# Kernel tuning notes

Hardware: AMD Instinct MI355X
Metric: run time of the kernel (lower is better)

## Reference

```python
import jax, jax.numpy as jnp
import numpy as np

N, K, E, H, I = 8192, 2, 8, 2048, 1408


def setup_inputs() -> dict:
    key = jax.random.key(0)
    k1, k2, k3, k4, k5 = jax.random.split(key, 5)
    x = jax.random.normal(k1, (N, H), dtype=jnp.float32)
    topk_indices = jax.random.randint(k2, (N, K), 0, E, dtype=jnp.int32)
    topk_weights = jax.random.uniform(k3, (N, K), dtype=jnp.float32)
    # normalize routing weights per token (typical top-k softmax output scale)
    topk_weights = topk_weights / jnp.sum(topk_weights, axis=-1, keepdims=True)
    scale = 0.02  # typical init std, keeps activations well-scaled
    gate_up_proj = jax.random.normal(k4, (E, H, 2 * I), dtype=jnp.float32) * scale
    down_proj = jax.random.normal(k5, (E, I, H), dtype=jnp.float32) * scale
    return {"x": x, "topk_indices": topk_indices, "topk_weights": topk_weights,
            "gate_up_proj": gate_up_proj, "down_proj": down_proj}


def reference(x, topk_indices, topk_weights, gate_up_proj, down_proj):
    """MoE experts: route -> grouped GEMM SwiGLU -> grouped GEMM -> weighted unroute.

    x: [N, H]; topk_indices/topk_weights: [N, K];
    gate_up_proj: [E, H, 2I]; down_proj: [E, I, H].
    """
    n, k = topk_indices.shape
    e = gate_up_proj.shape[0]
    flat_e = topk_indices.reshape(-1)                 # [N*K] expert id per routed slot
    sort_idx = jnp.argsort(flat_e)                    # stable sort: group slots by expert
    token_idx = sort_idx // k                         # source token for each sorted slot
    sorted_tokens = x[token_idx]                      # [N*K, H]
    group_sizes = jnp.bincount(flat_e, length=e).astype(jnp.int32)  # [E]
    # grouped (ragged) GEMM over contiguous expert groups
    h = jax.lax.ragged_dot(sorted_tokens, gate_up_proj, group_sizes)  # [N*K, 2I]
    gate_h, up_h = jnp.split(h, 2, axis=-1)
    intermediate = jax.nn.silu(gate_h) * up_h          # fused SwiGLU
    out_sorted = jax.lax.ragged_dot(intermediate, down_proj, group_sizes)  # [N*K, H]
    # weighted scatter-combine back to token order
    w_sorted = topk_weights.reshape(-1)[sort_idx]      # [N*K]
    out = jnp.zeros_like(x).at[token_idx].add(out_sorted * w_sorted[:, None])
    return out
```

## Files before the change

kernel.cpp:

```cpp
#include <hip/hip_runtime.h>


#define N_TOK 8192
#define TOPK  2
#define NEXP  8
#define HD    2048
#define ID    1408
#define NK    (N_TOK * TOPK)
#define NT256 (NK / 256 + NEXP)

typedef __bf16 bf16x8 __attribute__((ext_vector_type(8)));
typedef float  f32x4  __attribute__((ext_vector_type(4)));

__device__ __forceinline__ float b2f(unsigned short u) {
    union { unsigned int i; float f; } v; v.i = ((unsigned int)u) << 16; return v.f;
}
__device__ __forceinline__ unsigned short f2b(float f) {
    union { float f; unsigned int i; } v; v.f = f;
    unsigned int x = v.i;
    return (unsigned short)((x + 0x7fffu + ((x >> 16) & 1u)) >> 16);
}

__device__ __forceinline__ void glds16(const void* g, void* l) {
    __builtin_amdgcn_global_load_lds(
        (const __attribute__((address_space(1))) unsigned int*)g,
        (__attribute__((address_space(3))) unsigned int*)l,
        16, 0, 0);
}


__global__ void probe_k(const unsigned short* __restrict__ xu, int* __restrict__ mode) {
    __shared__ int c;
    if (threadIdx.x == 0) c = 0;
    __syncthreads();
    float a = fabsf(b2f(xu[threadIdx.x * 2]));
    int sane = (a > 1e-4f && a < 100.f) ? 1 : 0;
    atomicAdd(&c, sane);
    __syncthreads();
    if (threadIdx.x == 0) mode[0] = (c < 512) ? 1 : 0;
}


__global__ void convert_x(const void* __restrict__ x, unsigned short* __restrict__ xb,
                          const int* __restrict__ mode) {
    int gid = blockIdx.x * 256 + threadIdx.x;
    size_t o = (size_t)gid * 8;
    if (mode[0]) {
        const float* f = (const float*)x + o;
        float4 f0 = *(const float4*)f;
        float4 f1 = *(const float4*)(f + 4);
        uint4 v;
        v.x = f2b(f0.x) | ((unsigned int)f2b(f0.y) << 16);
        v.y = f2b(f0.z) | ((unsigned int)f2b(f0.w) << 16);
        v.z = f2b(f1.x) | ((unsigned int)f2b(f1.y) << 16);
        v.w = f2b(f1.z) | ((unsigned int)f2b(f1.w) << 16);
        *(uint4*)(xb + o) = v;
    } else {
        *(uint4*)(xb + o) = *(const uint4*)((const unsigned short*)x + o);
    }
}


__global__ void init_k(int* cnt, int* fill) {
    int t = threadIdx.x;
    if (t < NEXP) { cnt[t] = 0; fill[t] = 0; }
}

__global__ void route_count(const int* __restrict__ idx, int* __restrict__ cnt) {
    int s = blockIdx.x * 256 + threadIdx.x;
    if (s < NK) atomicAdd(&cnt[idx[s]], 1);
}

__global__ void route_scan(const int* __restrict__ cnt, int* __restrict__ base,
                           int* __restrict__ tb) {
    if (threadIdx.x == 0) {
        int acc = 0, tacc = 0;
        for (int e = 0; e < NEXP; e++) {
            base[e] = acc; tb[e] = tacc;
            acc += cnt[e]; tacc += (cnt[e] + 255) >> 8;
        }
        base[NEXP] = acc; tb[NEXP] = tacc;
    }
}

__global__ void route_scatter(const int* __restrict__ idx,
                              const int* __restrict__ base,
                              int* __restrict__ fill,
                              int* __restrict__ tok,
                              int* __restrict__ inv) {
    int s = blockIdx.x * 256 + threadIdx.x;
    if (s < NK) {
        int e = idx[s];
        int p = base[e] + atomicAdd(&fill[e], 1);
        tok[p] = s >> 1;
        inv[s] = p;
    }
}


__global__ void transpose_k(const void* __restrict__ in, unsigned short* __restrict__ out,
                            int R, int C, const int* __restrict__ mode) {
    __shared__ float tile[64][65];
    bool fp32m = (mode[0] != 0);
    int e  = blockIdx.z;
    int c0 = blockIdx.x * 64, r0 = blockIdx.y * 64;
    int t = threadIdx.x;
    if (fp32m) {
        const float* inp = (const float*)in + (size_t)e * R * C;
        for (int i = 0; i < 16; i++) {
            int lin = t + i * 256;
            int r = lin >> 6, c = lin & 63;
            tile[r][c] = inp[(size_t)(r0 + r) * C + c0 + c];
        }
    } else {
        const unsigned int* inp = (const unsigned int*)in + (size_t)e * R * (C >> 1);
        for (int i = 0; i < 8; i++) {
            int lin = t + i * 256;
            int r = lin >> 5, cu = lin & 31;
            unsigned int v = inp[(size_t)(r0 + r) * (C >> 1) + (c0 >> 1) + cu];
            tile[r][2 * cu]     = b2f((unsigned short)(v & 0xffffu));
            tile[r][2 * cu + 1] = b2f((unsigned short)(v >> 16));
        }
    }
    __syncthreads();
    unsigned int* outp = (unsigned int*)out + (size_t)e * C * (R >> 1);
    for (int i = 0; i < 8; i++) {
        int lin = t + i * 256;
        int c = lin >> 5, ru = lin & 31;
        unsigned int lo = f2b(tile[2 * ru][c]);
        unsigned int hi = f2b(tile[2 * ru + 1][c]);
        outp[(size_t)(c0 + c) * (R >> 1) + (r0 >> 1) + ru] = lo | (hi << 16);
    }
}



template<int KD, int ND, int LDA, bool GATHER>
__launch_bounds__(512, 2)
__global__ void gemm8_k(const unsigned short* __restrict__ A,
                        const unsigned short* __restrict__ B,
                        const int* __restrict__ base,
                        const int* __restrict__ tb,
                        const int* __restrict__ tok,
                        unsigned short* __restrict__ C) {
    extern __shared__ unsigned short lds[];
    const int CT = ND / 256;
    const int KT = KD / 64;
    int G = gridDim.x;
    int orig = blockIdx.x;
    int q8 = G >> 3, r8 = G & 7, xcd = orig & 7, lin = orig >> 3;
    int wgid = (xcd < r8 ? xcd * (q8 + 1) : r8 * (q8 + 1) + (xcd - r8) * q8) + lin;
    int ct  = wgid % CT;
    int rtf = wgid / CT;
    if (rtf >= tb[NEXP]) return;
    int e = 0;
    while (tb[e + 1] <= rtf) e++;
    int row0 = base[e] + (rtf - tb[e]) * 256;
    int rend = base[e + 1];

    int tid  = threadIdx.x;
    int lane = tid & 63;
    int wave = tid >> 6;
    int wm16 = (wave & 1) * 16;
    int wn16 = (wave >> 1) * 16;
    int l15 = lane & 15, qq = lane >> 4;
    int l7  = l15 & 7;

    const unsigned short* bbase = B + (size_t)e * ND * KD + (size_t)(ct * 256) * KD;

    const unsigned short* agp[2][2];
    const unsigned short* bgp[2][2];
    for (int j = 0; j < 2; j++) {
        int s = j * 512 + tid;
        int r = s >> 3;
        int c = (s & 7) ^ (r & 7);
        for (int h = 0; h < 2; h++) {
            int p = row0 + h * 128 + r;
            bool sv = (p < rend);
            const unsigned short* ar;
            if (GATHER) ar = sv ? A + (size_t)tok[p] * LDA : A;
            else        ar = sv ? A + (size_t)p * LDA      : A;
            agp[j][h] = ar + c * 8;
            bgp[j][h] = bbase + (size_t)(h * 128 + r) * KD + c * 8;
        }
    }
    int wbase = wave * 512;

    f32x4 acc[8][4];
#pragma unroll
    for (int m = 0; m < 8; m++)
#pragma unroll
        for (int n = 0; n < 4; n++) acc[m][n] = (f32x4){0.f, 0.f, 0.f, 0.f};

    bf16x8 af0[2], af1[2], bq[4][2];

#define STAGE_A(buf, h, kt) do { int _k = ((kt) < KT ? (kt) : KT - 1) * 64;     \
    glds16(agp[0][h] + _k, &lds[(buf) * 16384 + (h) * 8192 + wbase]);           \
    glds16(agp[1][h] + _k, &lds[(buf) * 16384 + (h) * 8192 + 4096 + wbase]); } while (0)
#define STAGE_B(buf, h, kt) do { int _k = ((kt) < KT ? (kt) : KT - 1) * 64;     \
    glds16(bgp[0][h] + _k, &lds[32768 + (buf) * 16384 + (h) * 8192 + wbase]);   \
    glds16(bgp[1][h] + _k, &lds[32768 + (buf) * 16384 + (h) * 8192 + 4096 + wbase]); } while (0)

#define ALDS(buf, m, ks) (*(const bf16x8*)&lds[(buf) * 16384 +                  \
    (((m) * 32 + wm16 + l15) * 8 + ((((ks) * 4) + qq) ^ l7)) * 8])
#define BLDS(buf, n, ks) (*(const bf16x8*)&lds[32768 + (buf) * 16384 +          \
    (((n) * 64 + wn16 + l15) * 8 + ((((ks) * 4) + qq) ^ l7)) * 8])

#define PH_READA(buf, m0)                                                       \
    af0[0] = ALDS(buf, m0, 0); af0[1] = ALDS(buf, m0, 1);                       \
    af1[0] = ALDS(buf, (m0) + 1, 0); af1[1] = ALDS(buf, (m0) + 1, 1);
#define PH_READB(buf)                                                           \
    _Pragma("unroll") for (int n = 0; n < 4; n++) {                             \
        bq[n][0] = BLDS(buf, n, 0); bq[n][1] = BLDS(buf, n, 1); }

#define MFMA16(m0) do {                                                         \
    _Pragma("unroll") for (int n = 0; n < 4; n++) {                             \
        acc[m0][n] = __builtin_amdgcn_mfma_f32_16x16x32_bf16(af0[0], bq[n][0], acc[m0][n], 0, 0, 0);         \
        acc[m0][n] = __builtin_amdgcn_mfma_f32_16x16x32_bf16(af0[1], bq[n][1], acc[m0][n], 0, 0, 0);         \
        acc[(m0) + 1][n] = __builtin_amdgcn_mfma_f32_16x16x32_bf16(af1[0], bq[n][0], acc[(m0) + 1][n], 0, 0, 0); \
        acc[(m0) + 1][n] = __builtin_amdgcn_mfma_f32_16x16x32_bf16(af1[1], bq[n][1], acc[(m0) + 1][n], 0, 0, 0); } } while (0)

#define SYNCA(m0)                                                               \
    __builtin_amdgcn_sched_barrier(0);                                          \
    __builtin_amdgcn_s_barrier();                                               \
    asm volatile("s_waitcnt lgkmcnt(0)" ::: "memory");                          \
    __builtin_amdgcn_sched_barrier(0);                                          \
    __builtin_amdgcn_s_setprio(1);                                              \
    MFMA16(m0);                                                                 \
    __builtin_amdgcn_s_setprio(0);                                              \
    __builtin_amdgcn_sched_barrier(0);                                          \
    __builtin_amdgcn_s_barrier();

#define SYNCV(m0)                                                               \
    __builtin_amdgcn_sched_barrier(0);                                          \
    asm volatile("s_waitcnt vmcnt(6)" ::: "memory");                            \
    __builtin_amdgcn_s_barrier();                                               \
    asm volatile("s_waitcnt lgkmcnt(0)" ::: "memory");                          \
    __builtin_amdgcn_sched_barrier(0);                                          \
    __builtin_amdgcn_s_setprio(1);                                              \
    MFMA16(m0);                                                                 \
    __builtin_amdgcn_s_setprio(0);                                              \
    __builtin_amdgcn_sched_barrier(0);                                          \
    __builtin_amdgcn_s_barrier();

    STAGE_A(0, 0, 0); STAGE_A(0, 1, 0); STAGE_B(0, 0, 0); STAGE_B(0, 1, 0);
    STAGE_B(1, 0, 1); STAGE_B(1, 1, 1); STAGE_A(1, 0, 1);
    __builtin_amdgcn_sched_barrier(0);
    asm volatile("s_waitcnt vmcnt(6)" ::: "memory");
    __builtin_amdgcn_s_barrier();
    __builtin_amdgcn_sched_barrier(0);

    for (int i = 0; i < KT / 2; i++) {
        int t1 = 2 * i + 1, t2 = 2 * i + 2, t3 = 2 * i + 3;
        PH_READB(0); PH_READA(0, 0); STAGE_A(1, 1, t1); SYNCA(0);
        PH_READA(0, 2);              STAGE_B(0, 0, t2); SYNCA(2);
        PH_READA(0, 4);              STAGE_B(0, 1, t2); SYNCA(4);
        PH_READA(0, 6);              STAGE_A(0, 0, t2); SYNCV(6);
        PH_READB(1); PH_READA(1, 0); STAGE_A(0, 1, t2); SYNCA(0);
        PH_READA(1, 2);              STAGE_B(1, 0, t3); SYNCA(2);
        PH_READA(1, 4);              STAGE_B(1, 1, t3); SYNCA(4);
        PH_READA(1, 6);              STAGE_A(1, 0, t3); SYNCV(6);
    }
    asm volatile("s_waitcnt vmcnt(0)" ::: "memory");

#undef STAGE_A
#undef STAGE_B
#undef ALDS
#undef BLDS
#undef PH_READA
#undef PH_READB
#undef MFMA16
#undef SYNCA
#undef SYNCV

#pragma unroll
    for (int m = 0; m < 8; m++) {
        int rbase = row0 + m * 32 + wm16 + qq * 4;
#pragma unroll
        for (int reg = 0; reg < 4; reg++) {
            int p = rbase + reg;
            if (p >= rend) continue;
#pragma unroll
            for (int n = 0; n < 4; n++) {
                int col = ct * 256 + n * 64 + wn16 + l15;
                C[(size_t)p * ND + col] = f2b(acc[m][n][reg]);
            }
        }
    }
}


__global__ void swiglu_k(unsigned short* __restrict__ h) {
    int gid = blockIdx.x * 256 + threadIdx.x;
    int row = gid / (ID / 8);
    int c8 = (gid - row * (ID / 8)) * 8;
    unsigned short* hr = h + (size_t)row * (2 * ID);
    uint4 gv = *(const uint4*)(hr + c8);
    uint4 uv = *(const uint4*)(hr + ID + c8);
    const unsigned short* ga = (const unsigned short*)&gv;
    const unsigned short* ua = (const unsigned short*)&uv;
    uint4 o;
    unsigned int* ro = (unsigned int*)&o;
    for (int i = 0; i < 4; i++) {
        float g0 = b2f(ga[2 * i]),     u0 = b2f(ua[2 * i]);
        float g1 = b2f(ga[2 * i + 1]), u1 = b2f(ua[2 * i + 1]);
        float s0 = (g0 / (1.f + __expf(-g0))) * u0;
        float s1 = (g1 / (1.f + __expf(-g1))) * u1;
        ro[i] = f2b(s0) | ((unsigned int)f2b(s1) << 16);
    }
    *(uint4*)(hr + c8) = o;
}


__global__ void combine_k(const unsigned short* __restrict__ outs,
                          const int* __restrict__ inv,
                          const void* __restrict__ w,
                          void* __restrict__ out,
                          const int* __restrict__ mode) {
    bool fp32m = (mode[0] != 0);
    int gid = blockIdx.x * 256 + threadIdx.x;
    int t  = gid >> 8;
    int c8 = (gid & 255) * 8;
    int p0 = inv[t * 2], p1 = inv[t * 2 + 1];
    float w0, w1;
    if (fp32m) {
        const float* wf = (const float*)w;
        w0 = wf[t * 2]; w1 = wf[t * 2 + 1];
    } else {
        const unsigned short* wu = (const unsigned short*)w;
        w0 = b2f(wu[t * 2]); w1 = b2f(wu[t * 2 + 1]);
    }
    uint4 v0 = *(const uint4*)(outs + (size_t)p0 * HD + c8);
    uint4 v1 = *(const uint4*)(outs + (size_t)p1 * HD + c8);
    const unsigned short* a = (const unsigned short*)&v0;
    const unsigned short* b = (const unsigned short*)&v1;
    float r[8];
    for (int i = 0; i < 8; i++) r[i] = w0 * b2f(a[i]) + w1 * b2f(b[i]);
    if (fp32m) {
        float* of = (float*)out + (size_t)t * HD + c8;
        *(float4*)of       = make_float4(r[0], r[1], r[2], r[3]);
        *(float4*)(of + 4) = make_float4(r[4], r[5], r[6], r[7]);
    } else {
        uint4 o;
        unsigned int* ro = (unsigned int*)&o;
        for (int i = 0; i < 4; i++)
            ro[i] = f2b(r[2 * i]) | ((unsigned int)f2b(r[2 * i + 1]) << 16);
        *(uint4*)((unsigned short*)out + (size_t)t * HD + c8) = o;
    }
}


extern "C" void kernel_launch(void* const* d_in, const int* in_sizes, int n_in,
                              void* d_out, int out_size, void* d_ws, size_t ws_size,
                              hipStream_t stream) {
    const void* x   = d_in[0];
    const int*  idx = (const int*)d_in[1];
    const void* w   = d_in[2];
    const void* gup = d_in[3];
    const void* dwn = d_in[4];

    char* ws = (char*)d_ws;
    int* mode = (int*)(ws);
    int* cnt  = (int*)(ws + 64);
    int* base = (int*)(ws + 128);
    int* fill = (int*)(ws + 192);
    int* tb   = (int*)(ws + 256);
    int* tok  = (int*)(ws + 512);
    int* inv  = (int*)(ws + 512 + 4 * NK);
    unsigned short* h    = (unsigned short*)(ws + 262144);
    unsigned short* xb   = h    + (size_t)NK * 2 * ID;
    unsigned short* dwnT = xb   + (size_t)N_TOK * HD;
    unsigned short* gupT = dwnT + (size_t)NEXP * HD * ID;
    unsigned short* outs = gupT;

    static bool attr_done = false;
    if (!attr_done) {
        hipFuncSetAttribute(
            reinterpret_cast<const void*>(&gemm8_k<HD, 2 * ID, HD, true>),
            hipFuncAttributeMaxDynamicSharedMemorySize, 131072);
        hipFuncSetAttribute(
            reinterpret_cast<const void*>(&gemm8_k<ID, HD, 2 * ID, false>),
            hipFuncAttributeMaxDynamicSharedMemorySize, 131072);
        attr_done = true;
    }

    probe_k<<<1, 1024, 0, stream>>>((const unsigned short*)x, mode);
    convert_x<<<(N_TOK * HD / 8) / 256, 256, 0, stream>>>(x, xb, mode);

    init_k<<<1, 64, 0, stream>>>(cnt, fill);
    route_count<<<NK / 256, 256, 0, stream>>>(idx, cnt);
    route_scan<<<1, 64, 0, stream>>>(cnt, base, tb);
    route_scatter<<<NK / 256, 256, 0, stream>>>(idx, base, fill, tok, inv);

    transpose_k<<<dim3(2 * ID / 64, HD / 64, NEXP), 256, 0, stream>>>(
        gup, gupT, HD, 2 * ID, mode);
    transpose_k<<<dim3(HD / 64, ID / 64, NEXP), 256, 0, stream>>>(
        dwn, dwnT, ID, HD, mode);

    gemm8_k<HD, 2 * ID, HD, true>
        <<<NT256 * (2 * ID / 256), 512, 131072, stream>>>(xb, gupT, base, tb, tok, h);
    swiglu_k<<<(NK * (ID / 8)) / 256, 256, 0, stream>>>(h);
    gemm8_k<ID, HD, 2 * ID, false>
        <<<NT256 * (HD / 256), 512, 131072, stream>>>(h, dwnT, base, tb, tok, outs);

    combine_k<<<(N_TOK * HD / 8) / 256, 256, 0, stream>>>(outs, inv, w, d_out, mode);
}
```

Baseline: 941.3 us.

## Fuse SwiGLU into gate-up GEMM epilogue via interleaved weight layout

The transpose of gate_up weights now interleaves gate and up columns in 64-wide blocks, so each 256-column GEMM tile holds matching gate and up columns. The first grouped GEMM applies SiLU(gate)*up in its epilogue and writes a half-width intermediate. This removes the separate swiglu kernel and the write and re-read of the full 2I-wide activation buffer. The down GEMM now reads the compact intermediate with leading dimension I. The tile-to-column mapping depends on I being a multiple of 64 and on 2I being a multiple of 256, which holds for I=1408.

```diff
diff --git a/kernel.cpp b/kernel.cpp
--- a/kernel.cpp
+++ b/kernel.cpp
@@ -99,7 +99,7 @@
 
 
 __global__ void transpose_k(const void* __restrict__ in, unsigned short* __restrict__ out,
-                            int R, int C, const int* __restrict__ mode) {
+                            int R, int C, int ilv, const int* __restrict__ mode) {
     __shared__ float tile[64][65];
     bool fp32m = (mode[0] != 0);
     int e  = blockIdx.z;
@@ -127,15 +127,19 @@
     for (int i = 0; i < 8; i++) {
         int lin = t + i * 256;
         int c = lin >> 5, ru = lin & 31;
+        int cc = c0 + c;
+        int orow = cc;
+        if (ilv) orow = (cc < ID) ? ((cc >> 6) * 128 + (cc & 63))
+                                  : (((cc - ID) >> 6) * 128 + 64 + ((cc - ID) & 63));
         unsigned int lo = f2b(tile[2 * ru][c]);
         unsigned int hi = f2b(tile[2 * ru + 1][c]);
-        outp[(size_t)(c0 + c) * (R >> 1) + (r0 >> 1) + ru] = lo | (hi << 16);
-    }
-}
-
-
-
-template<int KD, int ND, int LDA, bool GATHER>
+        outp[(size_t)orow * (R >> 1) + (r0 >> 1) + ru] = lo | (hi << 16);
+    }
+}
+
+
+
+template<int KD, int NBTOT, int LDA, bool GATHER, bool FUSE>
 __launch_bounds__(512, 2)
 __global__ void gemm8_k(const unsigned short* __restrict__ A,
                         const unsigned short* __restrict__ B,
@@ -144,7 +148,8 @@
                         const int* __restrict__ tok,
                         unsigned short* __restrict__ C) {
     extern __shared__ unsigned short lds[];
-    const int CT = ND / 256;
+    const int CT = NBTOT / 256;
+    const int NC = FUSE ? NBTOT / 2 : NBTOT;
     const int KT = KD / 64;
     int G = gridDim.x;
     int orig = blockIdx.x;
@@ -166,7 +171,7 @@
     int l15 = lane & 15, qq = lane >> 4;
     int l7  = l15 & 7;
 
-    const unsigned short* bbase = B + (size_t)e * ND * KD + (size_t)(ct * 256) * KD;
+    const unsigned short* bbase = B + (size_t)e * NBTOT * KD + (size_t)(ct * 256) * KD;
 
     const unsigned short* agp[2][2];
     const unsigned short* bgp[2][2];
@@ -280,35 +285,24 @@
         for (int reg = 0; reg < 4; reg++) {
             int p = rbase + reg;
             if (p >= rend) continue;
-#pragma unroll
-            for (int n = 0; n < 4; n++) {
-                int col = ct * 256 + n * 64 + wn16 + l15;
-                C[(size_t)p * ND + col] = f2b(acc[m][n][reg]);
+            if (FUSE) {
+#pragma unroll
+                for (int n2 = 0; n2 < 2; n2++) {
+                    float g = acc[m][2 * n2][reg];
+                    float u = acc[m][2 * n2 + 1][reg];
+                    float s = (g / (1.f + __expf(-g))) * u;
+                    int col = ct * 128 + n2 * 64 + wn16 + l15;
+                    C[(size_t)p * NC + col] = f2b(s);
+                }
+            } else {
+#pragma unroll
+                for (int n = 0; n < 4; n++) {
+                    int col = ct * 256 + n * 64 + wn16 + l15;
+                    C[(size_t)p * NC + col] = f2b(acc[m][n][reg]);
+                }
             }
         }
     }
-}
-
-
-__global__ void swiglu_k(unsigned short* __restrict__ h) {
-    int gid = blockIdx.x * 256 + threadIdx.x;
-    int row = gid / (ID / 8);
-    int c8 = (gid - row * (ID / 8)) * 8;
-    unsigned short* hr = h + (size_t)row * (2 * ID);
-    uint4 gv = *(const uint4*)(hr + c8);
-    uint4 uv = *(const uint4*)(hr + ID + c8);
-    const unsigned short* ga = (const unsigned short*)&gv;
-    const unsigned short* ua = (const unsigned short*)&uv;
-    uint4 o;
-    unsigned int* ro = (unsigned int*)&o;
-    for (int i = 0; i < 4; i++) {
-        float g0 = b2f(ga[2 * i]),     u0 = b2f(ua[2 * i]);
-        float g1 = b2f(ga[2 * i + 1]), u1 = b2f(ua[2 * i + 1]);
-        float s0 = (g0 / (1.f + __expf(-g0))) * u0;
-        float s1 = (g1 / (1.f + __expf(-g1))) * u1;
-        ro[i] = f2b(s0) | ((unsigned int)f2b(s1) << 16);
-    }
-    *(uint4*)(hr + c8) = o;
 }
 
 
@@ -367,19 +361,19 @@
     int* tb   = (int*)(ws + 256);
     int* tok  = (int*)(ws + 512);
     int* inv  = (int*)(ws + 512 + 4 * NK);
-    unsigned short* h    = (unsigned short*)(ws + 262144);
-    unsigned short* xb   = h    + (size_t)NK * 2 * ID;
-    unsigned short* dwnT = xb   + (size_t)N_TOK * HD;
-    unsigned short* gupT = dwnT + (size_t)NEXP * HD * ID;
-    unsigned short* outs = gupT;
+    unsigned short* inter = (unsigned short*)(ws + 262144);
+    unsigned short* xb    = inter + (size_t)NK * ID;
+    unsigned short* dwnT  = xb    + (size_t)N_TOK * HD;
+    unsigned short* gupT  = dwnT  + (size_t)NEXP * HD * ID;
+    unsigned short* outs  = gupT;
 
     static bool attr_done = false;
     if (!attr_done) {
         hipFuncSetAttribute(
-            reinterpret_cast<const void*>(&gemm8_k<HD, 2 * ID, HD, true>),
+            reinterpret_cast<const void*>(&gemm8_k<HD, 2 * ID, HD, true, true>),
             hipFuncAttributeMaxDynamicSharedMemorySize, 131072);
         hipFuncSetAttribute(
-            reinterpret_cast<const void*>(&gemm8_k<ID, HD, 2 * ID, false>),
+            reinterpret_cast<const void*>(&gemm8_k<ID, HD, ID, false, false>),
             hipFuncAttributeMaxDynamicSharedMemorySize, 131072);
         attr_done = true;
     }
@@ -393,15 +387,14 @@
     route_scatter<<<NK / 256, 256, 0, stream>>>(idx, base, fill, tok, inv);
 
     transpose_k<<<dim3(2 * ID / 64, HD / 64, NEXP), 256, 0, stream>>>(
-        gup, gupT, HD, 2 * ID, mode);
+        gup, gupT, HD, 2 * ID, 1, mode);
     transpose_k<<<dim3(HD / 64, ID / 64, NEXP), 256, 0, stream>>>(
-        dwn, dwnT, ID, HD, mode);
-
-    gemm8_k<HD, 2 * ID, HD, true>
-        <<<NT256 * (2 * ID / 256), 512, 131072, stream>>>(xb, gupT, base, tb, tok, h);
-    swiglu_k<<<(NK * (ID / 8)) / 256, 256, 0, stream>>>(h);
-    gemm8_k<ID, HD, 2 * ID, false>
-        <<<NT256 * (HD / 256), 512, 131072, stream>>>(h, dwnT, base, tb, tok, outs);
+        dwn, dwnT, ID, HD, 0, mode);
+
+    gemm8_k<HD, 2 * ID, HD, true, true>
+        <<<NT256 * (2 * ID / 256), 512, 131072, stream>>>(xb, gupT, base, tb, tok, inter);
+    gemm8_k<ID, HD, ID, false, false>
+        <<<NT256 * (HD / 256), 512, 131072, stream>>>(inter, dwnT, base, tb, tok, outs);
 
     combine_k<<<(N_TOK * HD / 8) / 256, 256, 0, stream>>>(outs, inv, w, d_out, mode);
 }
```

New measurement: 905.1 us. 3.8% less time.
